# Performance work log

Hardware: AMD Instinct MI355X
Metric: run time of the kernel (lower is better)

The kernel has to match this reference:

```python
import jax, jax.numpy as jnp
import numpy as np

B, S, H = 4, 2048, 1024
E, F = 8, 4096
K = 2  # hardcoded top-k in the original forward


def setup_inputs() -> dict:
    key = jax.random.key(0)
    ks = jax.random.split(key, 8)
    scale = 0.02
    x = jax.random.normal(ks[0], (B, S, H), dtype=jnp.float32)
    Wr = jax.random.normal(ks[1], (H, E), dtype=jnp.float32) * scale
    br = jnp.zeros((E,), dtype=jnp.float32)
    W1 = jax.random.normal(ks[2], (E, H, F), dtype=jnp.float32) * scale
    b1 = jnp.zeros((E, F), dtype=jnp.float32)
    W2 = jax.random.normal(ks[3], (E, F, H), dtype=jnp.float32) * scale
    b2 = jnp.zeros((E, H), dtype=jnp.float32)
    return {"x": x, "Wr": Wr, "br": br, "W1": W1, "b1": b1, "W2": W2, "b2": b2}


def reference(x, Wr, br, W1, b1, W2, b2):
    # Router: [B,S,H] @ [H,E] -> [B,S,E]
    router_logits = jnp.einsum('bsh,he->bse', x, Wr) + br
    router_probs = jax.nn.softmax(router_logits, axis=-1)
    top_k_probs, top_k_indices = jax.lax.top_k(router_probs, K)
    top_k_probs = top_k_probs / jnp.sum(top_k_probs, axis=-1, keepdims=True)
    # NOTE: original code weights EVERY selected expert by the normalized top-1 prob.
    p0 = top_k_probs[..., 0]  # [B,S]

    combined = jnp.zeros((B, S, H), dtype=x.dtype)
    for e in range(E):
        mask = jnp.any(top_k_indices == e, axis=-1)  # [B,S]
        # Dense FFN (dropout deterministic => identity); gelu approximate (flax default)
        h = jax.nn.gelu(jnp.einsum('bsh,hf->bsf', x, W1[e]) + b1[e])
        y = jnp.einsum('bsf,fh->bsh', h, W2[e]) + b2[e]
        combined = combined + jnp.where(mask[..., None], y * p0[..., None], 0.0)
    return combined
```

## Files before the change

kernel.cpp:

```cpp
#include <hip/hip_runtime.h>
#include <hip/hip_bf16.h>


typedef __bf16 bf16;
typedef __attribute__((ext_vector_type(4))) __bf16 bf16x4;
typedef __attribute__((ext_vector_type(8))) __bf16 bf16x8;
typedef __attribute__((ext_vector_type(4))) float f32x4;

#define GLD16(g, l) __builtin_amdgcn_global_load_lds( \
    (__attribute__((address_space(1))) void*)(g),      \
    (__attribute__((address_space(3))) void*)(l), 16, 0, 0)

__device__ __forceinline__ float gelu_fast(float v) {
  float u = v * fmaf(v * v, 0.0713548162726f, 1.5957691216057308f);
  return v * __builtin_amdgcn_rcpf(1.0f + __expf(-u));
}

__global__ __launch_bounds__(256) void router_kernel(
    const float* __restrict__ x, const float* __restrict__ Wr,
    const float* __restrict__ br, int* __restrict__ e01,
    float* __restrict__ p0arr) {
  int wv = threadIdx.x >> 6;
  int l = threadIdx.x & 63;
  int t = blockIdx.x * 4 + wv;
  float acc[8];
#pragma unroll
  for (int e = 0; e < 8; e++) acc[e] = 0.f;
  const float* xr = x + (size_t)t * 1024;
#pragma unroll
  for (int i = 0; i < 16; i++) {
    int h = l + i * 64;
    float xv = xr[h];
    const float4* w4 = (const float4*)(Wr + h * 8);
    float4 wa = w4[0], wb = w4[1];
    acc[0] += xv * wa.x; acc[1] += xv * wa.y; acc[2] += xv * wa.z; acc[3] += xv * wa.w;
    acc[4] += xv * wb.x; acc[5] += xv * wb.y; acc[6] += xv * wb.z; acc[7] += xv * wb.w;
  }
#pragma unroll
  for (int e = 0; e < 8; e++) {
    float v = acc[e];
#pragma unroll
    for (int m = 1; m < 64; m <<= 1) v += __shfl_xor(v, m, 64);
    acc[e] = v + br[e];
  }
  int i1 = 0; float m1 = acc[0];
#pragma unroll
  for (int e = 1; e < 8; e++) { if (acc[e] > m1) { m1 = acc[e]; i1 = e; } }
  int i2 = -1; float m2 = -3.4e38f;
#pragma unroll
  for (int e = 0; e < 8; e++) { if (e != i1 && acc[e] > m2) { m2 = acc[e]; i2 = e; } }
  if (l == 0) {
    e01[t] = i1 | (i2 << 8);
    p0arr[t] = 1.0f / (1.0f + __expf(m2 - m1));
  }
}

__global__ __launch_bounds__(1024) void slots_kernel(
    const int* __restrict__ e01, int* __restrict__ meta,
    int* __restrict__ slot1, int* __restrict__ slot2) {
  __shared__ int wtot[16];
  int tid = threadIdx.x;
  int l = tid & 63, wv = tid >> 6;
  int t0 = tid * 8;
  int i1[8], i2[8];
#pragma unroll
  for (int i = 0; i < 8; i++) {
    int ee = e01[t0 + i];
    i1[i] = ee & 255;
    i2[i] = (ee >> 8) & 255;
  }
  int offl[9];
  int running = 0;
  for (int e = 0; e < 8; e++) {
    offl[e] = running;
    int cthread = 0;
#pragma unroll
    for (int i = 0; i < 8; i++) cthread += (i1[i] == e) + (i2[i] == e);
    int inc = cthread;
#pragma unroll
    for (int d = 1; d < 64; d <<= 1) {
      int v = __shfl_up(inc, d, 64);
      if (l >= d) inc += v;
    }
    if (l == 63) wtot[wv] = inc;
    __syncthreads();
    int wbase = 0, total = 0;
#pragma unroll
    for (int w = 0; w < 16; w++) {
      int tw = wtot[w];
      wbase += (w < wv) ? tw : 0;
      total += tw;
    }
    int base = running + wbase + (inc - cthread);
#pragma unroll
    for (int i = 0; i < 8; i++) {
      if (i1[i] == e) { slot1[t0 + i] = base; base++; }
      if (i2[i] == e) { slot2[t0 + i] = base; base++; }
    }
    running += total;
    __syncthreads();
  }
  offl[8] = running;
  if (tid == 0) {
#pragma unroll
    for (int e = 0; e < 9; e++) meta[e] = offl[e];
    int nt = 0;
    for (int e = 0; e < 8; e++)
      for (int r = offl[e]; r < offl[e + 1]; r += 256)
        meta[16 + (nt++)] = r | (e << 20);
    meta[10] = nt;
  }
}

__global__ __launch_bounds__(256) void prep_kernel(
    const float* __restrict__ x, const int* __restrict__ slot1,
    const int* __restrict__ slot2, bf16* __restrict__ Xg,
    const float* __restrict__ W1, bf16* __restrict__ W1t,
    const float* __restrict__ W2, bf16* __restrict__ W2t) {
  __shared__ float tile[64][65];
  int b = blockIdx.x;
  if (b < 8192) {
    int t = b;
    int s1 = slot1[t], s2 = slot2[t];
    float4 v = ((const float4*)(x + (size_t)t * 1024))[threadIdx.x];
    bf16x4 bv = { (bf16)v.x, (bf16)v.y, (bf16)v.z, (bf16)v.w };
    *(bf16x4*)(Xg + (size_t)s1 * 1024 + threadIdx.x * 4) = bv;
    *(bf16x4*)(Xg + (size_t)s2 * 1024 + threadIdx.x * 4) = bv;
    return;
  }
  const float* in; bf16* outp; int R, C, bx, by, bz;
  if (b < 16384) {
    int b2 = b - 8192;
    in = W1; outp = W1t; R = 1024; C = 4096;
    bx = b2 & 63; by = (b2 >> 6) & 15; bz = b2 >> 10;
  } else {
    int b2 = b - 16384;
    in = W2; outp = W2t; R = 4096; C = 1024;
    bx = b2 & 15; by = (b2 >> 4) & 63; bz = b2 >> 10;
  }
  size_t base = (size_t)bz * R * C;
  int gr0 = by * 64, gc0 = bx * 64;
  int tr = threadIdx.x >> 4;
  int tc4 = (threadIdx.x & 15) * 4;
#pragma unroll
  for (int i = 0; i < 4; i++) {
    int r = tr + i * 16;
    float4 v = *(const float4*)&in[base + (size_t)(gr0 + r) * C + gc0 + tc4];
    tile[r][tc4] = v.x; tile[r][tc4 + 1] = v.y;
    tile[r][tc4 + 2] = v.z; tile[r][tc4 + 3] = v.w;
  }
  __syncthreads();
  int rr0 = (threadIdx.x & 7) * 8;
  int cc0 = threadIdx.x >> 3;
#pragma unroll
  for (int i = 0; i < 2; i++) {
    int cc = cc0 + i * 32;
    bf16x8 v;
#pragma unroll
    for (int k = 0; k < 8; k++) v[k] = (bf16)tile[rr0 + k][cc];
    *(bf16x8*)&outp[base + (size_t)(gc0 + cc) * R + gr0 + rr0] = v;
  }
}

__device__ __forceinline__ bool xcd_tile(int b, int ntiles, int nshift,
                                         int& m_idx, int& n_tile) {
  int xcd = b & 7, j = b >> 3;
  int total = ntiles << nshift;
  int q = total >> 3, r = total & 7;
  int cnt = q + (xcd < r ? 1 : 0);
  if (j >= cnt) return false;
  int start = (xcd < r) ? xcd * (q + 1) : r * (q + 1) + (xcd - r) * q;
  int tidx = start + j;
  m_idx = tidx >> nshift;
  n_tile = tidx & ((1 << nshift) - 1);
  return true;
}

__device__ __forceinline__ void gemm_core(
    const bf16* __restrict__ Abase, const bf16* __restrict__ Bbase,
    int K, int NT, char* smem, f32x4 acc[8][4], int wr, int wc, int l) {
  int tid = threadIdx.x;
  size_t K2 = (size_t)K * 2;
  const char* srcA[4]; const char* srcB[2];
  int dstA[4], dstB[2];
#pragma unroll
  for (int i = 0; i < 4; i++) {
    int byteoff = (tid + i * 256) * 16;
    int p = byteoff >> 7, W = byteoff & 127;
    int L = W ^ ((p & 7) << 4);
    int r = 2 * p + (L >> 6), c = L & 63;
    srcA[i] = (const char*)Abase + (size_t)r * K2 + c;
    dstA[i] = byteoff;
  }
#pragma unroll
  for (int i = 0; i < 2; i++) {
    int byteoff = (tid + i * 256) * 16;
    int p = byteoff >> 7, W = byteoff & 127;
    int L = W ^ ((p & 7) << 4);
    int r = 2 * p + (L >> 6), c = L & 63;
    srcB[i] = (const char*)Bbase + (size_t)r * K2 + c;
    dstB[i] = 16384 + byteoff;
  }
  int offA[8], offB[4];
  int kc16 = (l >> 4) << 4;
#pragma unroll
  for (int mf = 0; mf < 8; mf++) {
    int r = wr * 128 + mf * 16 + (l & 15);
    int p = r >> 1;
    offA[mf] = (p << 7) + ((((r & 1) << 6) | kc16) ^ ((p & 7) << 4));
  }
#pragma unroll
  for (int nf = 0; nf < 4; nf++) {
    int r = wc * 64 + nf * 16 + (l & 15);
    int p = r >> 1;
    offB[nf] = 16384 + (p << 7) + ((((r & 1) << 6) | kc16) ^ ((p & 7) << 4));
  }
#pragma unroll
  for (int t = 0; t < 2; t++) {
    char* bu = smem + t * 24576;
#pragma unroll
    for (int i = 0; i < 4; i++) GLD16(srcA[i] + t * 64, bu + dstA[i]);
#pragma unroll
    for (int i = 0; i < 2; i++) GLD16(srcB[i] + t * 64, bu + dstB[i]);
  }
  asm volatile("s_waitcnt vmcnt(6)" ::: "memory");
  __builtin_amdgcn_s_barrier();
  char* bc = smem;
  char* bs = smem + 2 * 24576;
  for (int t = 0; t < NT; t++) {
    bool st = (t + 2) < NT;
    bf16x8 bfr[4], af[4];
#pragma unroll
    for (int nf = 0; nf < 4; nf++) bfr[nf] = *(const bf16x8*)(bc + offB[nf]);
#pragma unroll
    for (int mf = 0; mf < 4; mf++) af[mf] = *(const bf16x8*)(bc + offA[mf]);
    if (st) {
#pragma unroll
      for (int i = 0; i < 4; i++)
        GLD16(srcA[i] + (size_t)(t + 2) * 64, bs + dstA[i]);
    }
    __builtin_amdgcn_s_barrier();
    asm volatile("s_waitcnt lgkmcnt(0)" ::: "memory");
    __builtin_amdgcn_s_setprio(1);
#pragma unroll
    for (int mf = 0; mf < 4; mf++)
#pragma unroll
      for (int nf = 0; nf < 4; nf++)
        acc[mf][nf] = __builtin_amdgcn_mfma_f32_16x16x32_bf16(bfr[nf], af[mf], acc[mf][nf], 0, 0, 0);
    __builtin_amdgcn_s_setprio(0);
    __builtin_amdgcn_s_barrier();
#pragma unroll
    for (int mf = 0; mf < 4; mf++) af[mf] = *(const bf16x8*)(bc + offA[mf + 4]);
    if (st) {
#pragma unroll
      for (int i = 0; i < 2; i++)
        GLD16(srcB[i] + (size_t)(t + 2) * 64, bs + dstB[i]);
    }
    __builtin_amdgcn_s_barrier();
    asm volatile("s_waitcnt lgkmcnt(0)" ::: "memory");
    __builtin_amdgcn_s_setprio(1);
#pragma unroll
    for (int mf = 0; mf < 4; mf++)
#pragma unroll
      for (int nf = 0; nf < 4; nf++)
        acc[mf + 4][nf] = __builtin_amdgcn_mfma_f32_16x16x32_bf16(bfr[nf], af[mf], acc[mf + 4][nf], 0, 0, 0);
    __builtin_amdgcn_s_setprio(0);
    if (st)              { asm volatile("s_waitcnt vmcnt(6)" ::: "memory"); }
    else if (t + 1 < NT) { asm volatile("s_waitcnt vmcnt(0)" ::: "memory"); }
    __builtin_amdgcn_s_barrier();
    bc += 24576; if (bc == smem + 73728) bc = smem;
    bs += 24576; if (bs == smem + 73728) bs = smem;
  }
}

__global__ __launch_bounds__(256, 2) void gemm1_kernel(
    const bf16* __restrict__ Xg, const bf16* __restrict__ W1t,
    const float* __restrict__ b1, bf16* __restrict__ hbuf,
    const int* __restrict__ meta) {
  __shared__ __align__(16) char smem[73728];
  int m_idx, n_tile;
  if (!xcd_tile(blockIdx.x, meta[10], 5, m_idx, n_tile)) return;
  int ti = meta[16 + m_idx];
  int row0 = ti & 0xFFFFF;
  int e = ti >> 20;
  int rowEnd = meta[1 + e];
  int tid = threadIdx.x;
  int w = tid >> 6, l = tid & 63;
  int wr = w >> 1, wc = w & 1;
  f32x4 acc[8][4];
#pragma unroll
  for (int a = 0; a < 8; a++)
#pragma unroll
    for (int bb = 0; bb < 4; bb++) acc[a][bb] = (f32x4){0.f, 0.f, 0.f, 0.f};
  gemm_core(Xg + (size_t)row0 * 1024,
            W1t + ((size_t)e * 4096 + n_tile * 128) * 1024,
            1024, 32, smem, acc, wr, wc, l);
  int mrow = l & 15, nq = (l >> 4) * 4;
  int gn0 = n_tile * 128 + wc * 64 + nq;
  f32x4 bv[4];
#pragma unroll
  for (int nf = 0; nf < 4; nf++)
    bv[nf] = *(const f32x4*)(b1 + e * 4096 + gn0 + nf * 16);
#pragma unroll
  for (int mf = 0; mf < 8; mf++) {
    int gm = row0 + wr * 128 + mf * 16 + mrow;
    if (gm < rowEnd) {
      bf16* rp = hbuf + (size_t)gm * 4096 + gn0;
#pragma unroll
      for (int nf = 0; nf < 4; nf++) {
        bf16x4 o;
#pragma unroll
        for (int jj = 0; jj < 4; jj++)
          o[jj] = (bf16)gelu_fast(acc[mf][nf][jj] + bv[nf][jj]);
        *(bf16x4*)(rp + nf * 16) = o;
      }
    }
  }
}

__global__ __launch_bounds__(256, 2) void gemm2_kernel(
    const bf16* __restrict__ hbuf, const bf16* __restrict__ W2t,
    const float* __restrict__ b2, bf16* __restrict__ yb,
    const int* __restrict__ meta) {
  __shared__ __align__(16) char smem[73728];
  int m_idx, n_tile;
  if (!xcd_tile(blockIdx.x, meta[10], 3, m_idx, n_tile)) return;
  int ti = meta[16 + m_idx];
  int row0 = ti & 0xFFFFF;
  int e = ti >> 20;
  int rowEnd = meta[1 + e];
  int tid = threadIdx.x;
  int w = tid >> 6, l = tid & 63;
  int wr = w >> 1, wc = w & 1;
  f32x4 acc[8][4];
#pragma unroll
  for (int a = 0; a < 8; a++)
#pragma unroll
    for (int bb = 0; bb < 4; bb++) acc[a][bb] = (f32x4){0.f, 0.f, 0.f, 0.f};
  gemm_core(hbuf + (size_t)row0 * 4096,
            W2t + ((size_t)e * 1024 + n_tile * 128) * 4096,
            4096, 128, smem, acc, wr, wc, l);
  int mrow = l & 15, nq = (l >> 4) * 4;
  int gn0 = n_tile * 128 + wc * 64 + nq;
  f32x4 bv[4];
#pragma unroll
  for (int nf = 0; nf < 4; nf++)
    bv[nf] = *(const f32x4*)(b2 + e * 1024 + gn0 + nf * 16);
#pragma unroll
  for (int mf = 0; mf < 8; mf++) {
    int gm = row0 + wr * 128 + mf * 16 + mrow;
    if (gm < rowEnd) {
      bf16* rp = yb + (size_t)gm * 1024 + gn0;
#pragma unroll
      for (int nf = 0; nf < 4; nf++) {
        bf16x4 o;
#pragma unroll
        for (int jj = 0; jj < 4; jj++)
          o[jj] = (bf16)(acc[mf][nf][jj] + bv[nf][jj]);
        *(bf16x4*)(rp + nf * 16) = o;
      }
    }
  }
}

__global__ __launch_bounds__(256) void combine_kernel(
    const bf16* __restrict__ yb, const int* __restrict__ slot1,
    const int* __restrict__ slot2, const float* __restrict__ p0arr,
    float* __restrict__ out) {
  int t = blockIdx.x;
  int s1 = slot1[t], s2 = slot2[t];
  float w0 = p0arr[t];
  bf16x4 a = *(const bf16x4*)(yb + (size_t)s1 * 1024 + threadIdx.x * 4);
  bf16x4 b = *(const bf16x4*)(yb + (size_t)s2 * 1024 + threadIdx.x * 4);
  float4 o;
  o.x = w0 * ((float)a[0] + (float)b[0]);
  o.y = w0 * ((float)a[1] + (float)b[1]);
  o.z = w0 * ((float)a[2] + (float)b[2]);
  o.w = w0 * ((float)a[3] + (float)b[3]);
  *(float4*)(out + (size_t)t * 1024 + threadIdx.x * 4) = o;
}

extern "C" void kernel_launch(void* const* d_in, const int* in_sizes, int n_in,
                              void* d_out, int out_size, void* d_ws, size_t ws_size,
                              hipStream_t stream) {
  const float* x  = (const float*)d_in[0];
  const float* Wr = (const float*)d_in[1];
  const float* br = (const float*)d_in[2];
  const float* W1 = (const float*)d_in[3];
  const float* b1 = (const float*)d_in[4];
  const float* W2 = (const float*)d_in[5];
  const float* b2 = (const float*)d_in[6];
  float* out = (float*)d_out;

  char* ws = (char*)d_ws;
  int*   meta  = (int*)(ws + 0);
  int*   e01   = (int*)(ws + 4096);
  float* p0    = (float*)(ws + 36864);
  int*   slot1 = (int*)(ws + 69632);
  int*   slot2 = (int*)(ws + 102400);
  bf16*  Xg    = (bf16*)(ws + 135168);
  bf16*  W1t   = (bf16*)(ws + 34213888ULL);
  bf16*  W2t   = (bf16*)(ws + 101322752ULL);
  bf16*  hb    = (bf16*)(ws + 168431616ULL);
  bf16*  yb    = Xg;

  router_kernel<<<2048, 256, 0, stream>>>(x, Wr, br, e01, p0);
  slots_kernel<<<1, 1024, 0, stream>>>(e01, meta, slot1, slot2);
  prep_kernel<<<24576, 256, 0, stream>>>(x, slot1, slot2, Xg, W1, W1t, W2, W2t);
  gemm1_kernel<<<2304, 256, 0, stream>>>(Xg, W1t, b1, hb, meta);
  gemm2_kernel<<<576, 256, 0, stream>>>(hb, W2t, b2, yb, meta);
  combine_kernel<<<8192, 256, 0, stream>>>(yb, slot1, slot2, p0, out);
}
```

Baseline: 734.1 us.

## Fuse weight fp32-to-bf16 transpose into GEMM B-tile loading

The separate prep pass that transposed and converted W1/W2 to bf16 is removed. Each GEMM now loads the fp32 weights directly through registers, converts them to bf16 and writes the swizzled B tile into LDS inside the pipelined loop. This saves a full read and write of both weight tensors plus a kernel launch. The cost is that weight tiles are re-read in fp32 by every M-tile (twice the bytes per read, strided loads) and the B path now uses register staging and VALU conversion instead of async global-to-LDS loads.

```diff
diff --git a/kernel.cpp b/kernel.cpp
--- a/kernel.cpp
+++ b/kernel.cpp
@@ -112,54 +112,15 @@
   }
 }
 
-__global__ __launch_bounds__(256) void prep_kernel(
+__global__ __launch_bounds__(256) void gather_kernel(
     const float* __restrict__ x, const int* __restrict__ slot1,
-    const int* __restrict__ slot2, bf16* __restrict__ Xg,
-    const float* __restrict__ W1, bf16* __restrict__ W1t,
-    const float* __restrict__ W2, bf16* __restrict__ W2t) {
-  __shared__ float tile[64][65];
-  int b = blockIdx.x;
-  if (b < 8192) {
-    int t = b;
-    int s1 = slot1[t], s2 = slot2[t];
-    float4 v = ((const float4*)(x + (size_t)t * 1024))[threadIdx.x];
-    bf16x4 bv = { (bf16)v.x, (bf16)v.y, (bf16)v.z, (bf16)v.w };
-    *(bf16x4*)(Xg + (size_t)s1 * 1024 + threadIdx.x * 4) = bv;
-    *(bf16x4*)(Xg + (size_t)s2 * 1024 + threadIdx.x * 4) = bv;
-    return;
-  }
-  const float* in; bf16* outp; int R, C, bx, by, bz;
-  if (b < 16384) {
-    int b2 = b - 8192;
-    in = W1; outp = W1t; R = 1024; C = 4096;
-    bx = b2 & 63; by = (b2 >> 6) & 15; bz = b2 >> 10;
-  } else {
-    int b2 = b - 16384;
-    in = W2; outp = W2t; R = 4096; C = 1024;
-    bx = b2 & 15; by = (b2 >> 4) & 63; bz = b2 >> 10;
-  }
-  size_t base = (size_t)bz * R * C;
-  int gr0 = by * 64, gc0 = bx * 64;
-  int tr = threadIdx.x >> 4;
-  int tc4 = (threadIdx.x & 15) * 4;
-#pragma unroll
-  for (int i = 0; i < 4; i++) {
-    int r = tr + i * 16;
-    float4 v = *(const float4*)&in[base + (size_t)(gr0 + r) * C + gc0 + tc4];
-    tile[r][tc4] = v.x; tile[r][tc4 + 1] = v.y;
-    tile[r][tc4 + 2] = v.z; tile[r][tc4 + 3] = v.w;
-  }
-  __syncthreads();
-  int rr0 = (threadIdx.x & 7) * 8;
-  int cc0 = threadIdx.x >> 3;
-#pragma unroll
-  for (int i = 0; i < 2; i++) {
-    int cc = cc0 + i * 32;
-    bf16x8 v;
-#pragma unroll
-    for (int k = 0; k < 8; k++) v[k] = (bf16)tile[rr0 + k][cc];
-    *(bf16x8*)&outp[base + (size_t)(gc0 + cc) * R + gr0 + rr0] = v;
-  }
+    const int* __restrict__ slot2, bf16* __restrict__ Xg) {
+  int t = blockIdx.x;
+  int s1 = slot1[t], s2 = slot2[t];
+  float4 v = ((const float4*)(x + (size_t)t * 1024))[threadIdx.x];
+  bf16x4 bv = { (bf16)v.x, (bf16)v.y, (bf16)v.z, (bf16)v.w };
+  *(bf16x4*)(Xg + (size_t)s1 * 1024 + threadIdx.x * 4) = bv;
+  *(bf16x4*)(Xg + (size_t)s2 * 1024 + threadIdx.x * 4) = bv;
 }
 
 __device__ __forceinline__ bool xcd_tile(int b, int ntiles, int nshift,
@@ -177,12 +138,12 @@
 }
 
 __device__ __forceinline__ void gemm_core(
-    const bf16* __restrict__ Abase, const bf16* __restrict__ Bbase,
+    const bf16* __restrict__ Abase, const float* __restrict__ Bw, int Nw,
     int K, int NT, char* smem, f32x4 acc[8][4], int wr, int wc, int l) {
   int tid = threadIdx.x;
   size_t K2 = (size_t)K * 2;
-  const char* srcA[4]; const char* srcB[2];
-  int dstA[4], dstB[2];
+  const char* srcA[4];
+  int dstA[4];
 #pragma unroll
   for (int i = 0; i < 4; i++) {
     int byteoff = (tid + i * 256) * 16;
@@ -192,15 +153,11 @@
     srcA[i] = (const char*)Abase + (size_t)r * K2 + c;
     dstA[i] = byteoff;
   }
-#pragma unroll
-  for (int i = 0; i < 2; i++) {
-    int byteoff = (tid + i * 256) * 16;
-    int p = byteoff >> 7, W = byteoff & 127;
-    int L = W ^ ((p & 7) << 4);
-    int r = 2 * p + (L >> 6), c = L & 63;
-    srcB[i] = (const char*)Bbase + (size_t)r * K2 + c;
-    dstB[i] = 16384 + byteoff;
-  }
+  int nloc = tid & 127, kh = tid >> 7;
+  const float* bcur = Bw + (size_t)(kh * 16) * Nw + nloc;
+  int pb = nloc >> 1;
+  int wb0 = 16384 + (pb << 7) + ((((nloc & 1) << 6) | (kh * 32)) ^ ((pb & 7) << 4));
+  int wb1 = wb0 ^ 16;
   int offA[8], offB[4];
   int kc16 = (l >> 4) << 4;
 #pragma unroll
@@ -215,15 +172,24 @@
     int p = r >> 1;
     offB[nf] = 16384 + (p << 7) + ((((r & 1) << 6) | kc16) ^ ((p & 7) << 4));
   }
+  float fb[16];
 #pragma unroll
   for (int t = 0; t < 2; t++) {
     char* bu = smem + t * 24576;
 #pragma unroll
+    for (int i = 0; i < 16; i++) fb[i] = bcur[(size_t)i * Nw];
+    __builtin_amdgcn_sched_barrier(0);
+#pragma unroll
     for (int i = 0; i < 4; i++) GLD16(srcA[i] + t * 64, bu + dstA[i]);
-#pragma unroll
-    for (int i = 0; i < 2; i++) GLD16(srcB[i] + t * 64, bu + dstB[i]);
-  }
-  asm volatile("s_waitcnt vmcnt(6)" ::: "memory");
+    __builtin_amdgcn_sched_barrier(0);
+    bf16x8 h0, h1;
+#pragma unroll
+    for (int i = 0; i < 8; i++) { h0[i] = (bf16)fb[i]; h1[i] = (bf16)fb[i + 8]; }
+    *(bf16x8*)(bu + wb0) = h0;
+    *(bf16x8*)(bu + wb1) = h1;
+    bcur += (size_t)32 * Nw;
+  }
+  asm volatile("s_waitcnt lgkmcnt(0)" ::: "memory");
   __builtin_amdgcn_s_barrier();
   char* bc = smem;
   char* bs = smem + 2 * 24576;
@@ -236,8 +202,12 @@
     for (int mf = 0; mf < 4; mf++) af[mf] = *(const bf16x8*)(bc + offA[mf]);
     if (st) {
 #pragma unroll
+      for (int i = 0; i < 16; i++) fb[i] = bcur[(size_t)i * Nw];
+      __builtin_amdgcn_sched_barrier(0);
+#pragma unroll
       for (int i = 0; i < 4; i++)
         GLD16(srcA[i] + (size_t)(t + 2) * 64, bs + dstA[i]);
+      __builtin_amdgcn_sched_barrier(0);
     }
     __builtin_amdgcn_s_barrier();
     asm volatile("s_waitcnt lgkmcnt(0)" ::: "memory");
@@ -251,11 +221,6 @@
     __builtin_amdgcn_s_barrier();
 #pragma unroll
     for (int mf = 0; mf < 4; mf++) af[mf] = *(const bf16x8*)(bc + offA[mf + 4]);
-    if (st) {
-#pragma unroll
-      for (int i = 0; i < 2; i++)
-        GLD16(srcB[i] + (size_t)(t + 2) * 64, bs + dstB[i]);
-    }
     __builtin_amdgcn_s_barrier();
     asm volatile("s_waitcnt lgkmcnt(0)" ::: "memory");
     __builtin_amdgcn_s_setprio(1);
@@ -265,8 +230,17 @@
       for (int nf = 0; nf < 4; nf++)
         acc[mf + 4][nf] = __builtin_amdgcn_mfma_f32_16x16x32_bf16(bfr[nf], af[mf], acc[mf + 4][nf], 0, 0, 0);
     __builtin_amdgcn_s_setprio(0);
-    if (st)              { asm volatile("s_waitcnt vmcnt(6)" ::: "memory"); }
-    else if (t + 1 < NT) { asm volatile("s_waitcnt vmcnt(0)" ::: "memory"); }
+    if (st) {
+      bf16x8 h0, h1;
+#pragma unroll
+      for (int i = 0; i < 8; i++) { h0[i] = (bf16)fb[i]; h1[i] = (bf16)fb[i + 8]; }
+      *(bf16x8*)(bs + wb0) = h0;
+      *(bf16x8*)(bs + wb1) = h1;
+      bcur += (size_t)32 * Nw;
+    } else if (t + 1 < NT) {
+      asm volatile("s_waitcnt vmcnt(0)" ::: "memory");
+    }
+    asm volatile("s_waitcnt lgkmcnt(0)" ::: "memory");
     __builtin_amdgcn_s_barrier();
     bc += 24576; if (bc == smem + 73728) bc = smem;
     bs += 24576; if (bs == smem + 73728) bs = smem;
@@ -274,7 +248,7 @@
 }
 
 __global__ __launch_bounds__(256, 2) void gemm1_kernel(
-    const bf16* __restrict__ Xg, const bf16* __restrict__ W1t,
+    const bf16* __restrict__ Xg, const float* __restrict__ W1,
     const float* __restrict__ b1, bf16* __restrict__ hbuf,
     const int* __restrict__ meta) {
   __shared__ __align__(16) char smem[73728];
@@ -293,7 +267,7 @@
 #pragma unroll
     for (int bb = 0; bb < 4; bb++) acc[a][bb] = (f32x4){0.f, 0.f, 0.f, 0.f};
   gemm_core(Xg + (size_t)row0 * 1024,
-            W1t + ((size_t)e * 4096 + n_tile * 128) * 1024,
+            W1 + (size_t)e * 1024 * 4096 + n_tile * 128, 4096,
             1024, 32, smem, acc, wr, wc, l);
   int mrow = l & 15, nq = (l >> 4) * 4;
   int gn0 = n_tile * 128 + wc * 64 + nq;
@@ -319,7 +293,7 @@
 }
 
 __global__ __launch_bounds__(256, 2) void gemm2_kernel(
-    const bf16* __restrict__ hbuf, const bf16* __restrict__ W2t,
+    const bf16* __restrict__ hbuf, const float* __restrict__ W2,
     const float* __restrict__ b2, bf16* __restrict__ yb,
     const int* __restrict__ meta) {
   __shared__ __align__(16) char smem[73728];
@@ -338,7 +312,7 @@
 #pragma unroll
     for (int bb = 0; bb < 4; bb++) acc[a][bb] = (f32x4){0.f, 0.f, 0.f, 0.f};
   gemm_core(hbuf + (size_t)row0 * 4096,
-            W2t + ((size_t)e * 1024 + n_tile * 128) * 4096,
+            W2 + (size_t)e * 4096 * 1024 + n_tile * 128, 1024,
             4096, 128, smem, acc, wr, wc, l);
   int mrow = l & 15, nq = (l >> 4) * 4;
   int gn0 = n_tile * 128 + wc * 64 + nq;
@@ -399,15 +373,13 @@
   int*   slot1 = (int*)(ws + 69632);
   int*   slot2 = (int*)(ws + 102400);
   bf16*  Xg    = (bf16*)(ws + 135168);
-  bf16*  W1t   = (bf16*)(ws + 34213888ULL);
-  bf16*  W2t   = (bf16*)(ws + 101322752ULL);
   bf16*  hb    = (bf16*)(ws + 168431616ULL);
   bf16*  yb    = Xg;
 
   router_kernel<<<2048, 256, 0, stream>>>(x, Wr, br, e01, p0);
   slots_kernel<<<1, 1024, 0, stream>>>(e01, meta, slot1, slot2);
-  prep_kernel<<<24576, 256, 0, stream>>>(x, slot1, slot2, Xg, W1, W1t, W2, W2t);
-  gemm1_kernel<<<2304, 256, 0, stream>>>(Xg, W1t, b1, hb, meta);
-  gemm2_kernel<<<576, 256, 0, stream>>>(hb, W2t, b2, yb, meta);
+  gather_kernel<<<8192, 256, 0, stream>>>(x, slot1, slot2, Xg);
+  gemm1_kernel<<<2304, 256, 0, stream>>>(Xg, W1, b1, hb, meta);
+  gemm2_kernel<<<576, 256, 0, stream>>>(hb, W2, b2, yb, meta);
   combine_kernel<<<8192, 256, 0, stream>>>(yb, slot1, slot2, p0, out);
 }
```

Measured after the change: 775.7 us. 5.7% more time.
